# Kernel tuning notes

Measured on AMD Instinct MI355X. Metric: run time of the kernel, lower is better.

## Reference

```python
import jax, jax.numpy as jnp
import numpy as np
from jax import lax

# Module constants (from init_kwargs)
B, C = 2, 64            # batch, in_channel
H, W, D = 64, 64, 64    # size
GROUPS = 2


def setup_inputs() -> dict:
    key = jax.random.key(0)
    ks = jax.random.split(key, 4)
    x = jax.random.normal(ks[0], (B, H * W * D, C), dtype=jnp.float32)
    # TransverseConv: Conv3d(2, W*2, (H,3,3), pad (0,1,1)) -> weight (O,I,kD,kH,kW)
    w_t = jax.random.normal(ks[1], (W * GROUPS, GROUPS, H, 3, 3), dtype=jnp.float32) * 0.02
    b_t = jnp.zeros((W * GROUPS,), jnp.float32)
    # CoronalConv: Conv3d(2, W*2, (3,3,D), pad (1,1,0))
    w_c = jax.random.normal(ks[2], (W * GROUPS, GROUPS, 3, 3, D), dtype=jnp.float32) * 0.02
    b_c = jnp.zeros((W * GROUPS,), jnp.float32)
    # map: Conv3d(2C, C, 1) stored as dense (C, 2C)
    w_map = jax.random.normal(ks[3], (C, 2 * C), dtype=jnp.float32) * 0.02
    b_map = jnp.zeros((C,), jnp.float32)
    return {"x": x, "w_t": w_t, "b_t": b_t, "w_c": w_c, "b_c": b_c,
            "w_map": w_map, "b_map": b_map}


def _forward(x, w_t, b_t, w_c, b_c, w_map, b_map):
    Bx, N, Cx = x.shape
    xg = x.transpose(0, 2, 1).reshape(Bx, Cx, H, W, D)   # (B,C,H,W,D)
    shortcut = xg
    xr = xg.reshape(Bx * Cx // GROUPS, GROUPS, H, W, D)
    dn = ('NCDHW', 'OIDHW', 'NCDHW')
    # Transverse: kernel spans full H -> output (B*C/2, 2W, 1, W, D)
    tans = lax.conv_general_dilated(xr, w_t, (1, 1, 1), [(0, 0), (1, 1), (1, 1)],
                                    dimension_numbers=dn)
    tans = tans + b_t[None, :, None, None, None]
    tans = tans.reshape(Bx, Cx, W, W, D)                 # (B,C,W,W,D)
    # Coronal: kernel spans full D -> output (B*C/2, 2W, H, W, 1)
    cor = lax.conv_general_dilated(xr, w_c, (1, 1, 1), [(1, 1), (1, 1), (0, 0)],
                                   dimension_numbers=dn)
    cor = cor + b_c[None, :, None, None, None]
    cor = cor.reshape(Bx, Cx, W, H, W)                   # (B,C,W,H,W)
    t1 = tans.transpose(0, 1, 3, 2, 4)                   # (B,C,W,W,D)
    c1 = cor.transpose(0, 1, 4, 3, 2)                    # (B,C,W,H,W)
    f = jnp.matmul(c1, t1).transpose(0, 1, 3, 2, 4)      # (B,C,H,W,D)
    attn = jnp.matmul(cor, tans).transpose(0, 1, 3, 2, 4)  # (B,C,H,W,D)
    cat = jnp.concatenate([shortcut * f, attn], axis=1)  # (B,2C,H,W,D)
    mapped = jnp.einsum('bkhwd,ck->bchwd', cat, w_map) + b_map[None, :, None, None, None]
    out = jax.nn.gelu(mapped, approximate=False)         # torch nn.GELU = exact erf
    return out.reshape(Bx, Cx, -1).transpose(0, 2, 1)    # (B,N,C)


def reference(x, w_t, b_t, w_c, b_c, w_map, b_map):
    return _forward(x, w_t, b_t, w_c, b_c, w_map, b_map)
```

## Files before the change

kernel.cpp:

```cpp
#include <hip/hip_runtime.h>
#include <hip/hip_bf16.h>
#include <math.h>

#define HWD 262144

typedef __attribute__((ext_vector_type(8))) short bf16x8;
typedef __attribute__((ext_vector_type(16))) float f32x16;

__device__ inline unsigned short bfu(float f) {
    __hip_bfloat16 h = __float2bfloat16(f);
    return *reinterpret_cast<unsigned short*>(&h);
}

__global__ void k_prep(const float* __restrict__ w_t, const float* __restrict__ w_c,
                       const float* __restrict__ w_map,
                       __hip_bfloat16* __restrict__ A_t, __hip_bfloat16* __restrict__ A_c,
                       __hip_bfloat16* __restrict__ Wb) {
    int i = blockIdx.x * 256 + threadIdx.x;
    if (i < 147456) {
        int kk = i & 15, oc = (i >> 4) & 127, ks = i >> 11;
        int z4 = ks & 3, kq = ks >> 2;
        int g = kq / 9, tap = kq - 9 * g;
        int z = z4 * 16 + kk;
        A_t[i] = __float2bfloat16(w_t[((oc * 2 + g) * 64 + z) * 9 + tap]);
        A_c[i] = __float2bfloat16(w_c[((oc * 2 + g) * 9 + tap) * 64 + z]);
    }
    if (i < 8192) {
        Wb[i] = __float2bfloat16(w_map[i]);
    }
}

__device__ inline void pack_row_bf16(__hip_bfloat16* dst, const float* src) {
    unsigned short u[16];
#pragma unroll
    for (int j = 0; j < 16; ++j) u[j] = bfu(src[j]);
    uint4* q = reinterpret_cast<uint4*>(dst);
    q[0] = *reinterpret_cast<const uint4*>(&u[0]);
    q[1] = *reinterpret_cast<const uint4*>(&u[8]);
}

__global__ void k_trans_c(const float* __restrict__ x, __hip_bfloat16* __restrict__ Xc) {
    __shared__ unsigned short tile[256][68];
    int b = blockIdx.y;
    long n0 = (long)blockIdx.x * 256;
    int t = threadIdx.x;
    const float4* xp4 = (const float4*)(x + ((long)b * HWD + n0) * 64);
#pragma unroll
    for (int i = 0; i < 16; ++i) {
        int f4i = i * 256 + t;
        float4 v = xp4[f4i];
        int nl = f4i >> 4, c4 = (f4i & 15) * 4;
        ushort4 u;
        u.x = bfu(v.x); u.y = bfu(v.y); u.z = bfu(v.z); u.w = bfu(v.w);
        *(ushort4*)&tile[nl][c4] = u;
    }
    __syncthreads();
    int c = t >> 2, hwl = t & 3;
    int hw0 = blockIdx.x * 4;
    __hip_bfloat16* dst0 = Xc + (long)(b * 64 + c) * HWD + (long)(hw0 + hwl) * 16;
#pragma unroll
    for (int z4 = 0; z4 < 4; ++z4) {
        unsigned short u[16];
#pragma unroll
        for (int j = 0; j < 16; ++j) u[j] = tile[hwl * 64 + z4 * 16 + j][c];
        __hip_bfloat16* dst = dst0 + z4 * 65536;
        *(uint4*)dst = *(const uint4*)&u[0];
        *(uint4*)(dst + 8) = *(const uint4*)&u[8];
    }
}

__global__ void k_trans_t(const float* __restrict__ x, __hip_bfloat16* __restrict__ Xt) {
    __shared__ unsigned short tile[256][68];
    int b = blockIdx.y;
    int wd0 = blockIdx.x * 4;
    int t = threadIdx.x;
    const float* xb = x + (long)b * HWD * 64 + (long)wd0 * 64;
#pragma unroll
    for (int i = 0; i < 16; ++i) {
        int idx = i * 256 + t;
        int h = idx >> 6, f = idx & 63;
        float4 v = *(const float4*)(xb + (long)h * 262144 + f * 4);
        int wdl = f >> 4, c4 = (f & 15) * 4;
        ushort4 u;
        u.x = bfu(v.x); u.y = bfu(v.y); u.z = bfu(v.z); u.w = bfu(v.w);
        *(ushort4*)&tile[wdl * 64 + h][c4] = u;
    }
    __syncthreads();
    int c = t >> 2, wdl = t & 3;
    __hip_bfloat16* dst0 = Xt + (long)(b * 64 + c) * HWD + (long)(wd0 + wdl) * 16;
#pragma unroll
    for (int z4 = 0; z4 < 4; ++z4) {
        unsigned short u[16];
#pragma unroll
        for (int j = 0; j < 16; ++j) u[j] = tile[wdl * 64 + z4 * 16 + j][c];
        __hip_bfloat16* dst = dst0 + z4 * 65536;
        *(uint4*)dst = *(const uint4*)&u[0];
        *(uint4*)(dst + 8) = *(const uint4*)&u[8];
    }
}

__global__ __launch_bounds__(256, 4) void k_conv_mfma(
        const __hip_bfloat16* __restrict__ X, const __hip_bfloat16* __restrict__ Aglob,
        const float* __restrict__ bias, float* __restrict__ Out) {
    int L = blockIdx.x;
    int grp = (L & 7) * 8 + ((L >> 3) >> 5);
    int pt = (L >> 3) & 31;
    int b = grp >> 5, ch = grp & 31;
    int p0 = pt * 2;
    const short* Xg = (const short*)(X + ((long)(b * 64 + 2 * ch)) * HWD);
    const short* Ag = (const short*)Aglob;
    int t = threadIdx.x;
    int lane = t & 63, wv = t >> 6;
    int O0 = (wv >> 1) * 64;
    int N0 = (wv & 1) * 64;
    int lrow = lane & 31, lq = lane >> 5;
    int pr = N0 >> 6;

    f32x16 acc00 = {0}, acc01 = {0}, acc10 = {0}, acc11 = {0};

    const short* Ap = Ag + (O0 + lrow) * 16 + lq * 8;
    const uint4 zero4 = {0u, 0u, 0u, 0u};

    for (int kq = 0; kq < 18; ++kq) {
        int g = (kq >= 9) ? 1 : 0;
        int tap = kq - 9 * g;
        int r = tap / 3, s = tap - 3 * r;
        int pp = p0 + pr + r - 1;
        bool pok = (unsigned)pp < 64u;
        int qq0 = lrow + s - 1;
        int qq1 = qq0 + 32;
        bool q0ok = (unsigned)qq0 < 64u;
        bool q1ok = (unsigned)qq1 < 64u;
        const short* xb = Xg + (long)g * HWD + pp * 1024 + lq * 8;
#pragma unroll
        for (int z4 = 0; z4 < 4; ++z4) {
            int ks = kq * 4 + z4;
            uint4 b0u = zero4, b1u = zero4;
            if (pok) {
                const short* xz = xb + z4 * 65536;
                if (q0ok) b0u = *(const uint4*)(xz + qq0 * 16);
                if (q1ok) b1u = *(const uint4*)(xz + qq1 * 16);
            }
            uint4 a0u = *(const uint4*)(Ap + ks * 2048);
            uint4 a1u = *(const uint4*)(Ap + ks * 2048 + 512);
            bf16x8 a0 = *(bf16x8*)&a0u;
            bf16x8 a1 = *(bf16x8*)&a1u;
            bf16x8 b0 = *(bf16x8*)&b0u;
            bf16x8 b1 = *(bf16x8*)&b1u;
            acc00 = __builtin_amdgcn_mfma_f32_32x32x16_bf16(a0, b0, acc00, 0, 0, 0);
            acc01 = __builtin_amdgcn_mfma_f32_32x32x16_bf16(a0, b1, acc01, 0, 0, 0);
            acc10 = __builtin_amdgcn_mfma_f32_32x32x16_bf16(a1, b0, acc10, 0, 0, 0);
            acc11 = __builtin_amdgcn_mfma_f32_32x32x16_bf16(a1, b1, acc11, 0, 0, 0);
        }
    }

    long base0 = ((long)(b * 64 + 2 * ch)) * HWD + (long)p0 * 64;
    int n0l = N0 + lrow, n1l = N0 + 32 + lrow;
    long noff0 = (long)(n0l >> 6) * 64 + (n0l & 63);
    long noff1 = (long)(n1l >> 6) * 64 + (n1l & 63);
#pragma unroll
    for (int reg = 0; reg < 16; ++reg) {
        int row = (reg & 3) + 8 * (reg >> 2) + 4 * lq;
        int oc0 = O0 + row, oc1 = O0 + 32 + row;
        long cb0 = base0 + (long)(oc0 >> 6) * HWD + (long)(oc0 & 63) * 4096;
        long cb1 = base0 + (long)(oc1 >> 6) * HWD + (long)(oc1 & 63) * 4096;
        float bs0 = bias[oc0], bs1 = bias[oc1];
        Out[cb0 + noff0] = acc00[reg] + bs0;
        Out[cb0 + noff1] = acc01[reg] + bs0;
        Out[cb1 + noff0] = acc10[reg] + bs1;
        Out[cb1 + noff1] = acc11[reg] + bs1;
    }
}

__global__ void k_attn(const float* __restrict__ Cc, const float* __restrict__ T,
                       __hip_bfloat16* __restrict__ At) {
    __shared__ float As[64][65];
    __shared__ float Bs[64][64];
    int bc = blockIdx.x >> 6, w2 = blockIdx.x & 63;
    const float* Ap = Cc + ((long)bc * 64 + w2) * 4096;
    const float* Bp = T + ((long)bc * 64 + w2) * 4096;
    int t = threadIdx.x;
#pragma unroll
    for (int e0 = 0; e0 < 4096; e0 += 256) {
        int e = e0 + t;
        int r = e >> 6, q = e & 63;
        As[r][q] = Ap[e];
        Bs[r][q] = Bp[e];
    }
    __syncthreads();
    int h = t >> 2, dg = (t & 3) * 16;
    f32x16 acc = {0};
    for (int k = 0; k < 64; ++k) {
        float a = As[h][k];
#pragma unroll
        for (int i = 0; i < 16; ++i)
            acc[i] = fmaf(a, Bs[k][dg + i], acc[i]);
    }
    float tmp[16];
#pragma unroll
    for (int i = 0; i < 16; ++i) tmp[i] = acc[i];
    pack_row_bf16(At + (long)bc * HWD + (long)h * 4096 + w2 * 64 + dg, tmp);
}

__global__ __launch_bounds__(512, 4) void k_f(const float* __restrict__ Cc,
        const float* __restrict__ T, __hip_bfloat16* __restrict__ F) {
    __shared__ float As[16][64][8];
    __shared__ float Bs[16][8][68];
    int L = blockIdx.x;
    int xcd = L & 7, j = L >> 3;
    int bc = xcd * 16 + (j >> 3), wt = j & 7;
    const float* Ab = Cc + (long)bc * HWD + wt * 8;
    const float* Bb = T + (long)bc * HWD + wt * 8 * 64;
    int t = threadIdx.x;
    int w = t & 7, h = t >> 3;
    f32x16 acc0 = {0}, acc1 = {0}, acc2 = {0}, acc3 = {0};

    for (int w2c = 0; w2c < 4; ++w2c) {
        __syncthreads();
#pragma unroll
        for (int i = 0; i < 4; ++i) {
            int f = i * 512 + t;
            int half = f & 1, hh = (f >> 1) & 63, kk = f >> 7;
            float4 v = *(const float4*)(Ab + (long)(w2c * 16 + kk) * 4096 + hh * 64 + half * 4);
            *(float4*)&As[kk][hh][half * 4] = v;
        }
#pragma unroll
        for (int i = 0; i < 4; ++i) {
            int f = i * 512 + t;
            int d4 = f & 15, ww = (f >> 4) & 7, kk = f >> 7;
            float4 v = *(const float4*)(Bb + (long)(w2c * 16 + kk) * 4096 + ww * 64 + d4 * 4);
            *(float4*)&Bs[kk][ww][d4 * 4] = v;
        }
        __syncthreads();
        for (int kk = 0; kk < 16; ++kk) {
            float a = As[kk][h][w];
            const float* br = &Bs[kk][w][0];
#pragma unroll
            for (int i = 0; i < 16; ++i) {
                acc0[i] = fmaf(a, br[i], acc0[i]);
                acc1[i] = fmaf(a, br[16 + i], acc1[i]);
                acc2[i] = fmaf(a, br[32 + i], acc2[i]);
                acc3[i] = fmaf(a, br[48 + i], acc3[i]);
            }
        }
    }
    __hip_bfloat16* Fp = F + (long)bc * HWD + (long)h * 4096 + (wt * 8 + w) * 64;
    float tmp[16];
#pragma unroll
    for (int i = 0; i < 16; ++i) tmp[i] = acc0[i];
    pack_row_bf16(Fp, tmp);
#pragma unroll
    for (int i = 0; i < 16; ++i) tmp[i] = acc1[i];
    pack_row_bf16(Fp + 16, tmp);
#pragma unroll
    for (int i = 0; i < 16; ++i) tmp[i] = acc2[i];
    pack_row_bf16(Fp + 32, tmp);
#pragma unroll
    for (int i = 0; i < 16; ++i) tmp[i] = acc3[i];
    pack_row_bf16(Fp + 48, tmp);
}

__global__ __launch_bounds__(256, 4) void k_map(const float* __restrict__ x,
        const __hip_bfloat16* __restrict__ F, const __hip_bfloat16* __restrict__ At,
        const __hip_bfloat16* __restrict__ Wb, const float* __restrict__ b_map,
        float* __restrict__ out) {
    __shared__ float xs[16][257];
    __shared__ __hip_bfloat16 fa[16][264];
    __shared__ short Pl[256][24];
    __shared__ short Wt[64][136];

    int t = threadIdx.x;
    long n0 = (long)blockIdx.x * 256;
    int b = (int)(n0 >> 18);
    long nn0 = n0 & (HWD - 1);
    const float* xblk = x + n0 * 64;
    const __hip_bfloat16* Fb = F + (long)b * 64 * HWD + nn0;
    const __hip_bfloat16* Ab = At + (long)b * 64 * HWD + nn0;

#pragma unroll
    for (int i = 0; i < 4; ++i) {
        int e = i * 256 + t;
        int c = e >> 4, kk = (e & 15) * 8;
        *(uint4*)&Wt[c][kk] = *(const uint4*)((const short*)Wb + c * 128 + kk);
    }

    int lane = t & 63, wv = t >> 6;
    int lrow = lane & 31, lhalf = lane >> 5;
    f32x16 acc00 = {0}, acc01 = {0}, acc10 = {0}, acc11 = {0};

    for (int kc = 0; kc < 8; ++kc) {
        __syncthreads();
        if (kc < 4) {
#pragma unroll
            for (int i2 = 0; i2 < 4; ++i2) {
                int f = i2 * 256 + t;
                int nr = f >> 2, j4 = (f & 3) * 4;
                float4 v = *(const float4*)(xblk + nr * 64 + kc * 16 + j4);
                xs[j4 + 0][nr] = v.x;
                xs[j4 + 1][nr] = v.y;
                xs[j4 + 2][nr] = v.z;
                xs[j4 + 3][nr] = v.w;
            }
#pragma unroll
            for (int it = 0; it < 2; ++it) {
                int idx = it * 256 + t;
                int row = idx >> 5, seg = idx & 31;
                *(uint4*)&fa[row][seg * 8] =
                    *(const uint4*)(Fb + (long)(kc * 16 + row) * HWD + seg * 8);
            }
        } else {
#pragma unroll
            for (int it = 0; it < 2; ++it) {
                int idx = it * 256 + t;
                int row = idx >> 5, seg = idx & 31;
                *(uint4*)&fa[row][seg * 8] =
                    *(const uint4*)(Ab + (long)((kc - 4) * 16 + row) * HWD + seg * 8);
            }
        }
        __syncthreads();
        unsigned short pv[16];
        if (kc < 4) {
#pragma unroll
            for (int k2 = 0; k2 < 16; ++k2) {
                float p = xs[k2][t] * __bfloat162float(fa[k2][t]);
                pv[k2] = bfu(p);
            }
        } else {
#pragma unroll
            for (int k2 = 0; k2 < 16; ++k2)
                pv[k2] = *reinterpret_cast<const unsigned short*>(&fa[k2][t]);
        }
        *(uint4*)&Pl[t][0] = *(uint4*)&pv[0];
        *(uint4*)&Pl[t][8] = *(uint4*)&pv[8];
        __syncthreads();
        bf16x8 a0 = *(const bf16x8*)&Pl[wv * 64 + lrow][lhalf * 8];
        bf16x8 a1 = *(const bf16x8*)&Pl[wv * 64 + 32 + lrow][lhalf * 8];
        bf16x8 b0 = *(const bf16x8*)&Wt[lrow][kc * 16 + lhalf * 8];
        bf16x8 b1 = *(const bf16x8*)&Wt[32 + lrow][kc * 16 + lhalf * 8];
        acc00 = __builtin_amdgcn_mfma_f32_32x32x16_bf16(a0, b0, acc00, 0, 0, 0);
        acc01 = __builtin_amdgcn_mfma_f32_32x32x16_bf16(a0, b1, acc01, 0, 0, 0);
        acc10 = __builtin_amdgcn_mfma_f32_32x32x16_bf16(a1, b0, acc10, 0, 0, 0);
        acc11 = __builtin_amdgcn_mfma_f32_32x32x16_bf16(a1, b1, acc11, 0, 0, 0);
    }

    float bs0 = b_map[lrow];
    float bs1 = b_map[32 + lrow];
    const float inv_sqrt2 = 0.70710678118654752440f;
    float* ob = out + (n0 + wv * 64) * 64;
#pragma unroll
    for (int reg = 0; reg < 16; ++reg) {
        int nrow = (reg & 3) + 8 * (reg >> 2) + 4 * lhalf;
        float v00 = acc00[reg] + bs0;
        float v01 = acc01[reg] + bs1;
        float v10 = acc10[reg] + bs0;
        float v11 = acc11[reg] + bs1;
        v00 = 0.5f * v00 * (1.f + erff(v00 * inv_sqrt2));
        v01 = 0.5f * v01 * (1.f + erff(v01 * inv_sqrt2));
        v10 = 0.5f * v10 * (1.f + erff(v10 * inv_sqrt2));
        v11 = 0.5f * v11 * (1.f + erff(v11 * inv_sqrt2));
        ob[(long)nrow * 64 + lrow] = v00;
        ob[(long)nrow * 64 + 32 + lrow] = v01;
        ob[(long)(32 + nrow) * 64 + lrow] = v10;
        ob[(long)(32 + nrow) * 64 + 32 + lrow] = v11;
    }
}

extern "C" void kernel_launch(void* const* d_in, const int* in_sizes, int n_in,
                              void* d_out, int out_size, void* d_ws, size_t ws_size,
                              hipStream_t stream) {
    const float* x     = (const float*)d_in[0];
    const float* w_t   = (const float*)d_in[1];
    const float* b_t   = (const float*)d_in[2];
    const float* w_c   = (const float*)d_in[3];
    const float* b_c   = (const float*)d_in[4];
    const float* w_map = (const float*)d_in[5];
    const float* b_map = (const float*)d_in[6];
    float* out = (float*)d_out;
    float* ws = (float*)d_ws;

    __hip_bfloat16* Xc = (__hip_bfloat16*)ws;
    __hip_bfloat16* Xt = (__hip_bfloat16*)(ws + 16777216L);
    float* T = ws + 33554432L;
    float* Cc = out;
    __hip_bfloat16* A_t = (__hip_bfloat16*)(ws + 67108864L);
    __hip_bfloat16* A_c = (__hip_bfloat16*)(ws + 67182592L);
    __hip_bfloat16* Wb = (__hip_bfloat16*)(ws + 67256320L);
    __hip_bfloat16* At_bf = Xc;
    __hip_bfloat16* F_bf = Xt;

    hipLaunchKernelGGL(k_prep, dim3(576), dim3(256), 0, stream, w_t, w_c, w_map, A_t, A_c, Wb);
    hipLaunchKernelGGL(k_trans_c, dim3(1024, 2), dim3(256), 0, stream, x, Xc);
    hipLaunchKernelGGL(k_trans_t, dim3(1024, 2), dim3(256), 0, stream, x, Xt);
    hipLaunchKernelGGL(k_conv_mfma, dim3(2048), dim3(256), 0, stream, Xt, A_t, b_t, T);
    hipLaunchKernelGGL(k_conv_mfma, dim3(2048), dim3(256), 0, stream, Xc, A_c, b_c, Cc);
    hipLaunchKernelGGL(k_attn, dim3(8192), dim3(256), 0, stream, Cc, T, At_bf);
    hipLaunchKernelGGL(k_f, dim3(1024), dim3(512), 0, stream, Cc, T, F_bf);
    hipLaunchKernelGGL(k_map, dim3(2048), dim3(256), 0, stream, x, F_bf, At_bf, Wb, b_map, out);
}
```

Measured before the change: 822.1 us.

## Software-pipeline conv MFMA loads and give attention threads two rows each

The conv MFMA kernel now double-buffers its fragment loads, fetching the next tap's A/B fragments into registers while MFMAs run on the current ones. Its launch bounds drop to 2 blocks per SIMD to make room for the extra registers. The attention kernel switches to 128 threads, each computing two output rows with float4 global loads, so every B-row read from LDS is reused twice. This trades occupancy for latency hiding and register reuse.

```diff
diff --git a/kernel.cpp b/kernel.cpp
--- a/kernel.cpp
+++ b/kernel.cpp
@@ -99,7 +99,9 @@
     }
 }
 
-__global__ __launch_bounds__(256, 4) void k_conv_mfma(
+struct Frag { uint4 a0[4], a1[4], b0[4], b1[4]; };
+
+__global__ __launch_bounds__(256, 2) void k_conv_mfma(
         const __hip_bfloat16* __restrict__ X, const __hip_bfloat16* __restrict__ Aglob,
         const float* __restrict__ bias, float* __restrict__ Out) {
     int L = blockIdx.x;
@@ -119,39 +121,49 @@
     f32x16 acc00 = {0}, acc01 = {0}, acc10 = {0}, acc11 = {0};
 
     const short* Ap = Ag + (O0 + lrow) * 16 + lq * 8;
+    const short* XgL = Xg + lrow * 16 + lq * 8;
     const uint4 zero4 = {0u, 0u, 0u, 0u};
 
-    for (int kq = 0; kq < 18; ++kq) {
+    auto loadKq = [&](int kq, Frag& f) {
         int g = (kq >= 9) ? 1 : 0;
         int tap = kq - 9 * g;
         int r = tap / 3, s = tap - 3 * r;
         int pp = p0 + pr + r - 1;
         bool pok = (unsigned)pp < 64u;
-        int qq0 = lrow + s - 1;
-        int qq1 = qq0 + 32;
-        bool q0ok = (unsigned)qq0 < 64u;
-        bool q1ok = (unsigned)qq1 < 64u;
-        const short* xb = Xg + (long)g * HWD + pp * 1024 + lq * 8;
+        bool q0ok = pok && ((s > 0) || (lrow != 0));
+        bool q1ok = pok && ((s < 2) || (lrow != 31));
+        const short* px = XgL + ((long)g * HWD + pp * 1024 + (s - 1) * 16);
 #pragma unroll
         for (int z4 = 0; z4 < 4; ++z4) {
             int ks = kq * 4 + z4;
-            uint4 b0u = zero4, b1u = zero4;
-            if (pok) {
-                const short* xz = xb + z4 * 65536;
-                if (q0ok) b0u = *(const uint4*)(xz + qq0 * 16);
-                if (q1ok) b1u = *(const uint4*)(xz + qq1 * 16);
-            }
-            uint4 a0u = *(const uint4*)(Ap + ks * 2048);
-            uint4 a1u = *(const uint4*)(Ap + ks * 2048 + 512);
-            bf16x8 a0 = *(bf16x8*)&a0u;
-            bf16x8 a1 = *(bf16x8*)&a1u;
-            bf16x8 b0 = *(bf16x8*)&b0u;
-            bf16x8 b1 = *(bf16x8*)&b1u;
+            f.b0[z4] = q0ok ? *(const uint4*)(px + z4 * 65536) : zero4;
+            f.b1[z4] = q1ok ? *(const uint4*)(px + z4 * 65536 + 512) : zero4;
+            f.a0[z4] = *(const uint4*)(Ap + ks * 2048);
+            f.a1[z4] = *(const uint4*)(Ap + ks * 2048 + 512);
+        }
+    };
+    auto mfmaKq = [&](Frag& f) {
+#pragma unroll
+        for (int z4 = 0; z4 < 4; ++z4) {
+            bf16x8 a0 = *(bf16x8*)&f.a0[z4];
+            bf16x8 a1 = *(bf16x8*)&f.a1[z4];
+            bf16x8 b0 = *(bf16x8*)&f.b0[z4];
+            bf16x8 b1 = *(bf16x8*)&f.b1[z4];
             acc00 = __builtin_amdgcn_mfma_f32_32x32x16_bf16(a0, b0, acc00, 0, 0, 0);
             acc01 = __builtin_amdgcn_mfma_f32_32x32x16_bf16(a0, b1, acc01, 0, 0, 0);
             acc10 = __builtin_amdgcn_mfma_f32_32x32x16_bf16(a1, b0, acc10, 0, 0, 0);
             acc11 = __builtin_amdgcn_mfma_f32_32x32x16_bf16(a1, b1, acc11, 0, 0, 0);
         }
+    };
+
+    Frag fA, fB;
+    loadKq(0, fA);
+#pragma unroll
+    for (int k2 = 0; k2 < 9; ++k2) {
+        loadKq(2 * k2 + 1, fB);
+        mfmaKq(fA);
+        if (2 * k2 + 2 < 18) loadKq(2 * k2 + 2, fA);
+        mfmaKq(fB);
     }
 
     long base0 = ((long)(b * 64 + 2 * ch)) * HWD + (long)p0 * 64;
@@ -172,34 +184,44 @@
     }
 }
 
-__global__ void k_attn(const float* __restrict__ Cc, const float* __restrict__ T,
-                       __hip_bfloat16* __restrict__ At) {
+__global__ __launch_bounds__(128) void k_attn(const float* __restrict__ Cc,
+        const float* __restrict__ T, __hip_bfloat16* __restrict__ At) {
     __shared__ float As[64][65];
     __shared__ float Bs[64][64];
     int bc = blockIdx.x >> 6, w2 = blockIdx.x & 63;
-    const float* Ap = Cc + ((long)bc * 64 + w2) * 4096;
-    const float* Bp = T + ((long)bc * 64 + w2) * 4096;
-    int t = threadIdx.x;
-#pragma unroll
-    for (int e0 = 0; e0 < 4096; e0 += 256) {
-        int e = e0 + t;
-        int r = e >> 6, q = e & 63;
-        As[r][q] = Ap[e];
-        Bs[r][q] = Bp[e];
+    const float4* Ap4 = (const float4*)(Cc + ((long)bc * 64 + w2) * 4096);
+    const float4* Bp4 = (const float4*)(T + ((long)bc * 64 + w2) * 4096);
+    int t = threadIdx.x;
+#pragma unroll
+    for (int i = 0; i < 8; ++i) {
+        int f = i * 128 + t;
+        int r = f >> 4, q4 = (f & 15) * 4;
+        float4 v = Ap4[f];
+        As[r][q4 + 0] = v.x; As[r][q4 + 1] = v.y; As[r][q4 + 2] = v.z; As[r][q4 + 3] = v.w;
+        float4 w = Bp4[f];
+        *(float4*)&Bs[r][q4] = w;
     }
     __syncthreads();
-    int h = t >> 2, dg = (t & 3) * 16;
-    f32x16 acc = {0};
+    int h2 = t >> 2, dg = (t & 3) * 16;
+    f32x16 acc0 = {0}, acc1 = {0};
     for (int k = 0; k < 64; ++k) {
-        float a = As[h][k];
-#pragma unroll
-        for (int i = 0; i < 16; ++i)
-            acc[i] = fmaf(a, Bs[k][dg + i], acc[i]);
+        float a0 = As[h2][k];
+        float a1 = As[h2 + 32][k];
+        const float* br = &Bs[k][dg];
+#pragma unroll
+        for (int i = 0; i < 16; ++i) {
+            acc0[i] = fmaf(a0, br[i], acc0[i]);
+            acc1[i] = fmaf(a1, br[i], acc1[i]);
+        }
     }
     float tmp[16];
-#pragma unroll
-    for (int i = 0; i < 16; ++i) tmp[i] = acc[i];
-    pack_row_bf16(At + (long)bc * HWD + (long)h * 4096 + w2 * 64 + dg, tmp);
+    __hip_bfloat16* Ab = At + (long)bc * HWD + (long)h2 * 4096 + w2 * 64 + dg;
+#pragma unroll
+    for (int i = 0; i < 16; ++i) tmp[i] = acc0[i];
+    pack_row_bf16(Ab, tmp);
+#pragma unroll
+    for (int i = 0; i < 16; ++i) tmp[i] = acc1[i];
+    pack_row_bf16(Ab + 32L * 4096, tmp);
 }
 
 __global__ __launch_bounds__(512, 4) void k_f(const float* __restrict__ Cc,
@@ -393,7 +415,7 @@
     hipLaunchKernelGGL(k_trans_t, dim3(1024, 2), dim3(256), 0, stream, x, Xt);
     hipLaunchKernelGGL(k_conv_mfma, dim3(2048), dim3(256), 0, stream, Xt, A_t, b_t, T);
     hipLaunchKernelGGL(k_conv_mfma, dim3(2048), dim3(256), 0, stream, Xc, A_c, b_c, Cc);
-    hipLaunchKernelGGL(k_attn, dim3(8192), dim3(256), 0, stream, Cc, T, At_bf);
+    hipLaunchKernelGGL(k_attn, dim3(8192), dim3(128), 0, stream, Cc, T, At_bf);
     hipLaunchKernelGGL(k_f, dim3(1024), dim3(512), 0, stream, Cc, T, F_bf);
     hipLaunchKernelGGL(k_map, dim3(2048), dim3(256), 0, stream, x, F_bf, At_bf, Wb, b_map, out);
 }
```

Result: faster. 802.1 us (-2.4%).
